# Performance work log

Hardware: AMD Instinct MI355X
Metric: run time of the kernel (lower is better)

Reference implementation:

```python
import jax, jax.numpy as jnp
import numpy as np

D_MODEL, N_HEAD, HEAD_SIZE = 1024, 16, 64
NEG_INF = -1e30


def setup_inputs() -> dict:
    key = jax.random.key(0)
    ks = jax.random.split(key, 12)
    B, S = 4, 4096
    w = 0.02
    return {
        "query": jax.random.normal(ks[0], (B, S, D_MODEL), jnp.float32),
        "key":   jax.random.normal(ks[1], (B, S, D_MODEL), jnp.float32),
        "value": jax.random.normal(ks[2], (B, S, D_MODEL), jnp.float32),
        "mask":  jnp.ones((HEAD_SIZE, HEAD_SIZE), jnp.int32),
        "Wq": jax.random.normal(ks[3], (D_MODEL, HEAD_SIZE), jnp.float32) * w,
        "bq": jnp.zeros((HEAD_SIZE,), jnp.float32),
        "Wk": jax.random.normal(ks[4], (D_MODEL, HEAD_SIZE), jnp.float32) * w,
        "bk": jnp.zeros((HEAD_SIZE,), jnp.float32),
        "Wv": jax.random.normal(ks[5], (D_MODEL, HEAD_SIZE), jnp.float32) * w,
        "bv": jnp.zeros((HEAD_SIZE,), jnp.float32),
        "Wp": jax.random.normal(ks[6], (D_MODEL, D_MODEL), jnp.float32) * w,
        "bp": jnp.zeros((D_MODEL,), jnp.float32),
    }


def reference(query, key, value, mask, Wq, bq, Wk, bk, Wv, bv, Wp, bp):
    h, dh = N_HEAD, HEAD_SIZE
    # Linear projections: (B,S,d_model) -> (B,S,head_size)
    q = query @ Wq + bq
    k = key @ Wk + bk
    v = value @ Wv + bv
    # Faithful to torch: view(-1, h, dh).transpose(1,2) on (B,S,head_size)
    # -> (N, dh, h) with N = B*S/h
    q = q.reshape(-1, h, dh).transpose(0, 2, 1)
    k = k.reshape(-1, h, dh).transpose(0, 2, 1)
    v = v.reshape(-1, h, dh).transpose(0, 2, 1)
    scale = q.shape[-1] ** (-0.5)  # dhead = h in the original code
    # scores: (N, dh, dh)
    scores = jnp.einsum('nik,njk->nij', q, k) * scale
    scores = jnp.where(mask == 0, NEG_INF, scores)
    # NOTE: original code computes softmax(scores) but then overwrites it;
    # the actual output uses dropout(raw scores) @ v. Dropout in eval = identity.
    x = jnp.einsum('nij,njh->nih', scores, v)  # (N, dh, h)
    x = x.transpose(0, 2, 1).reshape(-1, h * dh)  # (N, d_model)
    return x @ Wp + bp
```

## Files before the change

kernel.cpp:

```cpp
#include <hip/hip_runtime.h>
#include <hip/hip_bf16.h>
#include <stdint.h>


typedef float f32x4 __attribute__((ext_vector_type(4)));
typedef short s16x8 __attribute__((ext_vector_type(8)));

#define T_TOK 16384
#define KDIM  1024
#define HS    64

__device__ __forceinline__ short f2bf(float f) {
    union { float f; uint32_t u; } x; x.f = f;
    uint32_t u = x.u;
    u += 0x7FFFu + ((u >> 16) & 1u);
    return (short)(u >> 16);
}

__device__ __forceinline__ void gl2lds16(const void* g, void* l) {
    __builtin_amdgcn_global_load_lds(
        (const __attribute__((address_space(1))) void*)g,
        (__attribute__((address_space(3))) void*)l, 16, 0, 0);
}

__global__ __launch_bounds__(256) void wtrans_kernel(
    const float* __restrict__ Wq, const float* __restrict__ Wk,
    const float* __restrict__ Wv, const float* __restrict__ Wp,
    short* __restrict__ Wtq, short* __restrict__ Wtk,
    short* __restrict__ Wtv, short* __restrict__ Wpt)
{
    const int bid = blockIdx.x;
    const float* src; short* dst; int N, k0, n0;
    if (bid < 256) { src = Wp; dst = Wpt; N = 1024; k0 = (bid >> 4) * 64; n0 = (bid & 15) * 64; }
    else {
        int r = bid - 256; int p = r >> 4;
        src = (p == 0) ? Wq : (p == 1) ? Wk : Wv;
        dst = (p == 0) ? Wtq : (p == 1) ? Wtk : Wtv;
        N = 64; k0 = (r & 15) * 64; n0 = 0;
    }
    __shared__ float Ts[64][68];
    const int tid = threadIdx.x;
    #pragma unroll
    for (int i = 0; i < 4; ++i) {
        int idx = i * 256 + tid;
        int r = idx >> 4, c4 = idx & 15;
        f32x4 v = *(const f32x4*)&src[(size_t)(k0 + r) * N + n0 + c4 * 4];
        *(f32x4*)&Ts[r][c4 * 4] = v;
    }
    __syncthreads();
    #pragma unroll
    for (int i = 0; i < 2; ++i) {
        int idx = i * 256 + tid;
        int n = idx >> 3, c8 = idx & 7;
        s16x8 h;
        #pragma unroll
        for (int j = 0; j < 8; ++j) h[j] = f2bf(Ts[c8 * 8 + j][n]);
        *(s16x8*)&dst[(size_t)(n0 + n) * KDIM + k0 + c8 * 8] = h;
    }
}

__global__ __launch_bounds__(256) void qkv_proj_kernel(
    const float* __restrict__ Q, const float* __restrict__ K,
    const float* __restrict__ V,
    const short* __restrict__ Wtq, const short* __restrict__ Wtk,
    const short* __restrict__ Wtv,
    const float* __restrict__ bq, const float* __restrict__ bk,
    const float* __restrict__ bv,
    float* __restrict__ OutQKV)
{
    const int p = blockIdx.y;
    const float* In = (p == 0) ? Q : (p == 1) ? K : V;
    const short* Wt = (p == 0) ? Wtq : (p == 1) ? Wtk : Wtv;
    const float* bb = (p == 0) ? bq : (p == 1) ? bk : bv;
    float* Out = OutQKV + (size_t)p * T_TOK * HS;

    __shared__ __align__(16) char ldsA[2][4096];
    __shared__ __align__(16) char ldsB[2][8192];

    const int tid  = threadIdx.x;
    const int wave = tid >> 6;
    const int lane = tid & 63;
    const int lhi  = lane >> 4;
    const int llo  = lane & 15;
    const int t0   = blockIdx.x * 32;

    int oB0 = (wave * 2 + 0) * 1024 + lane * 16;
    int oB1 = (wave * 2 + 1) * 1024 + lane * 16;
    int rB0 = oB0 >> 7, qB0 = (oB0 >> 4) & 7;
    int rB1 = oB1 >> 7, qB1 = (oB1 >> 4) & 7;
    size_t gB0 = (size_t)rB0 * KDIM + ((qB0 ^ (rB0 & 7)) * 8);
    size_t gB1 = (size_t)rB1 * KDIM + ((qB1 ^ (rB1 & 7)) * 8);

    const int rt = tid >> 3;
    const int dg = tid & 7;
    const float* gAp = In + (size_t)(t0 + rt) * KDIM + dg * 8;
    const int aWoff = rt * 128 + ((dg ^ (rt & 7)) * 16);

    f32x4 acc[2] = {};
    f32x4 ra[2][2];

    #define STAGE_B(b, kk) do {                              \
        gl2lds16(Wt + gB0 + (kk), &ldsB[b][oB0]);            \
        gl2lds16(Wt + gB1 + (kk), &ldsB[b][oB1]);            \
    } while (0)

    #define LOADA(s, kk) do {                                \
        ra[s][0] = *(const f32x4*)(gAp + (kk));              \
        ra[s][1] = *(const f32x4*)(gAp + (kk) + 4);          \
    } while (0)

    #define WRITEA(b, s) do {                                \
        s16x8 h;                                             \
        h[0] = f2bf(ra[s][0].x); h[1] = f2bf(ra[s][0].y);    \
        h[2] = f2bf(ra[s][0].z); h[3] = f2bf(ra[s][0].w);    \
        h[4] = f2bf(ra[s][1].x); h[5] = f2bf(ra[s][1].y);    \
        h[6] = f2bf(ra[s][1].z); h[7] = f2bf(ra[s][1].w);    \
        *(s16x8*)&ldsA[b][aWoff] = h;                        \
    } while (0)

    LOADA(0, 0);
    STAGE_B(0, 0);
    WRITEA(0, 0);
    LOADA(1, 64);

    #pragma unroll
    for (int c = 0; c < 16; ++c) {
        __syncthreads();
        if (c < 15) STAGE_B((c + 1) & 1, (c + 1) * 64);
        if (c < 14) LOADA(c & 1, (c + 2) * 64);
        if (c < 15) WRITEA((c + 1) & 1, (c + 1) & 1);
        const char* Ab = (const char*)ldsA[c & 1];
        const char* Bb = (const char*)ldsB[c & 1];
        #pragma unroll
        for (int hh = 0; hh < 2; ++hh) {
            int pf = (hh * 4 + lhi) ^ (llo & 7);
            s16x8 bf = *(const s16x8*)(Bb + (wave * 16 + llo) * 128 + pf * 16);
            #pragma unroll
            for (int tt = 0; tt < 2; ++tt) {
                int r = tt * 16 + llo;
                s16x8 af = *(const s16x8*)(Ab + r * 128 + pf * 16);
                acc[tt] = __builtin_amdgcn_mfma_f32_16x16x32_bf16(af, bf, acc[tt], 0, 0, 0);
            }
        }
    }
    #undef STAGE_B
    #undef LOADA
    #undef WRITEA

    const float bias = bb[wave * 16 + llo];
    #pragma unroll
    for (int tt = 0; tt < 2; ++tt)
        #pragma unroll
        for (int r = 0; r < 4; ++r)
            Out[(size_t)(t0 + tt * 16 + lhi * 4 + r) * HS + wave * 16 + llo] = acc[tt][r] + bias;
}

__global__ __launch_bounds__(256) void group_attn_kernel(
    const float* __restrict__ QKV, short* __restrict__ Xbf)
{
    const int n = blockIdx.x;
    __shared__ float Sq[16][68];
    __shared__ float Sk[16][68];
    __shared__ float Sv[16][68];
    __shared__ float KV[16][17];

    const int tid = threadIdx.x;
    const float* qp = QKV + (size_t)n * 16 * HS;
    const float* kp = qp + (size_t)T_TOK * HS;
    const float* vp = kp + (size_t)T_TOK * HS;

    {
        int row = tid >> 4, c4 = (tid & 15) * 4;
        *(f32x4*)&Sq[row][c4] = *(const f32x4*)&qp[tid * 4];
        *(f32x4*)&Sk[row][c4] = *(const f32x4*)&kp[tid * 4];
        *(f32x4*)&Sv[row][c4] = *(const f32x4*)&vp[tid * 4];
    }
    __syncthreads();

    {
        int b = tid >> 4, a = tid & 15;
        const f32x4* kb = (const f32x4*)&Sk[b][0];
        const f32x4* va = (const f32x4*)&Sv[a][0];
        float s = 0.f;
        #pragma unroll
        for (int j = 0; j < 16; ++j) {
            f32x4 x = kb[j], y = va[j];
            s += x.x * y.x + x.y * y.y + x.z * y.z + x.w * y.w;
        }
        KV[b][a] = s * 0.25f;
    }
    __syncthreads();

    const int i = tid & 63;
    const int w = tid >> 6;
    float qv[16];
    #pragma unroll
    for (int b = 0; b < 16; ++b) qv[b] = Sq[b][i];
    #pragma unroll
    for (int u = 0; u < 4; ++u) {
        int a = u * 4 + w;
        float s = 0.f;
        #pragma unroll
        for (int b = 0; b < 16; ++b) s += qv[b] * KV[b][a];
        Xbf[(size_t)n * 1024 + a * 64 + i] = f2bf(s);
    }
}

__global__ __launch_bounds__(256) void out_proj_kernel(
    const short* __restrict__ Xbf, const short* __restrict__ Wpt,
    const float* __restrict__ bp, float* __restrict__ Out)
{
    __shared__ __align__(16) char lds[2][12288];

    const int tid  = threadIdx.x;
    const int wave = tid >> 6;
    const int lane = tid & 63;
    const int lhi  = lane >> 4, llo = lane & 15;
    const int n0   = blockIdx.x * 64;
    const int m0   = blockIdx.y * 32;

    int oA = wave * 1024 + lane * 16;
    int rA = oA >> 7, qA = (oA >> 4) & 7;
    size_t gA = (size_t)(m0 + rA) * KDIM + ((qA ^ (rA & 7)) * 8);
    int oB0 = (wave * 2 + 0) * 1024 + lane * 16;
    int oB1 = (wave * 2 + 1) * 1024 + lane * 16;
    int rB0 = oB0 >> 7, qB0 = (oB0 >> 4) & 7;
    int rB1 = oB1 >> 7, qB1 = (oB1 >> 4) & 7;
    size_t gB0 = (size_t)(n0 + rB0) * KDIM + ((qB0 ^ (rB0 & 7)) * 8);
    size_t gB1 = (size_t)(n0 + rB1) * KDIM + ((qB1 ^ (rB1 & 7)) * 8);

    f32x4 acc[2] = {};

    #define STAGE3(b, kk) do {                                    \
        gl2lds16(Xbf + gA  + (kk), &lds[b][oA]);                  \
        gl2lds16(Wpt + gB0 + (kk), &lds[b][4096 + oB0]);          \
        gl2lds16(Wpt + gB1 + (kk), &lds[b][4096 + oB1]);          \
    } while (0)

    STAGE3(0, 0);
    for (int c = 0; c < 16; ++c) {
        __syncthreads();
        if (c < 15) STAGE3((c + 1) & 1, (c + 1) * 64);
        const char* Ab = lds[c & 1];
        const char* Bb = lds[c & 1] + 4096;
        #pragma unroll
        for (int hh = 0; hh < 2; ++hh) {
            int pB = (hh * 4 + lhi) ^ (llo & 7);
            s16x8 bf = *(const s16x8*)(Bb + (wave * 16 + llo) * 128 + pB * 16);
            #pragma unroll
            for (int tt = 0; tt < 2; ++tt) {
                int r = tt * 16 + llo;
                int pA = (hh * 4 + lhi) ^ (llo & 7);
                s16x8 af = *(const s16x8*)(Ab + r * 128 + pA * 16);
                acc[tt] = __builtin_amdgcn_mfma_f32_16x16x32_bf16(af, bf, acc[tt], 0, 0, 0);
            }
        }
    }
    #undef STAGE3

    const float bias = bp[n0 + wave * 16 + llo];
    #pragma unroll
    for (int tt = 0; tt < 2; ++tt)
        #pragma unroll
        for (int r = 0; r < 4; ++r)
            Out[(size_t)(m0 + tt * 16 + lhi * 4 + r) * KDIM + n0 + wave * 16 + llo]
                = acc[tt][r] + bias;
}

extern "C" void kernel_launch(void* const* d_in, const int* in_sizes, int n_in,
                              void* d_out, int out_size, void* d_ws, size_t ws_size,
                              hipStream_t stream) {
    const float* Q  = (const float*)d_in[0];
    const float* K  = (const float*)d_in[1];
    const float* V  = (const float*)d_in[2];
    const float* Wq = (const float*)d_in[4];
    const float* bq = (const float*)d_in[5];
    const float* Wk = (const float*)d_in[6];
    const float* bk = (const float*)d_in[7];
    const float* Wv = (const float*)d_in[8];
    const float* bv = (const float*)d_in[9];
    const float* Wp = (const float*)d_in[10];
    const float* bp = (const float*)d_in[11];
    float* out = (float*)d_out;

    char* ws = (char*)d_ws;
    float* qkv = (float*)ws;
    size_t off = (size_t)3 * T_TOK * HS * sizeof(float);
    short* Xbf = (short*)(ws + off); off += (size_t)1024 * 1024 * 2;
    short* Wtq = (short*)(ws + off); off += (size_t)HS * KDIM * 2;
    short* Wtk = (short*)(ws + off); off += (size_t)HS * KDIM * 2;
    short* Wtv = (short*)(ws + off); off += (size_t)HS * KDIM * 2;
    short* Wpt = (short*)(ws + off); off += (size_t)KDIM * KDIM * 2;

    wtrans_kernel<<<dim3(304), 256, 0, stream>>>(Wq, Wk, Wv, Wp, Wtq, Wtk, Wtv, Wpt);
    qkv_proj_kernel<<<dim3(T_TOK / 32, 3), 256, 0, stream>>>(
        Q, K, V, Wtq, Wtk, Wtv, bq, bk, bv, qkv);
    group_attn_kernel<<<dim3(1024), 256, 0, stream>>>(qkv, Xbf);
    out_proj_kernel<<<dim3(16, 32), 256, 0, stream>>>(Xbf, Wpt, bp, out);
}
```

Measured before the change: 252.9 us.

## Drop LDS staging in projection GEMMs and load MFMA fragments straight from global

Both the QKV projection and output projection kernels stop staging tiles through double-buffered shared memory with barriers. Each wave instead loads its A and B fragments directly from global memory into registers, and the block tile grows to 64 rows. The aim is to remove LDS traffic and __syncthreads overhead in these memory-bound GEMMs. In exchange there is no explicit prefetch pipelining, B fragments are loaded redundantly by every wave (relying on cache), and the grids shrink, which lowers parallelism.

```diff
diff --git a/kernel.cpp b/kernel.cpp
--- a/kernel.cpp
+++ b/kernel.cpp
@@ -15,12 +15,6 @@
     uint32_t u = x.u;
     u += 0x7FFFu + ((u >> 16) & 1u);
     return (short)(u >> 16);
-}
-
-__device__ __forceinline__ void gl2lds16(const void* g, void* l) {
-    __builtin_amdgcn_global_load_lds(
-        (const __attribute__((address_space(1))) void*)g,
-        (__attribute__((address_space(3))) void*)l, 16, 0, 0);
 }
 
 __global__ __launch_bounds__(256) void wtrans_kernel(
@@ -74,85 +68,51 @@
     const float* bb = (p == 0) ? bq : (p == 1) ? bk : bv;
     float* Out = OutQKV + (size_t)p * T_TOK * HS;
 
-    __shared__ __align__(16) char ldsA[2][4096];
-    __shared__ __align__(16) char ldsB[2][8192];
-
     const int tid  = threadIdx.x;
     const int wave = tid >> 6;
     const int lane = tid & 63;
     const int lhi  = lane >> 4;
     const int llo  = lane & 15;
-    const int t0   = blockIdx.x * 32;
-
-    int oB0 = (wave * 2 + 0) * 1024 + lane * 16;
-    int oB1 = (wave * 2 + 1) * 1024 + lane * 16;
-    int rB0 = oB0 >> 7, qB0 = (oB0 >> 4) & 7;
-    int rB1 = oB1 >> 7, qB1 = (oB1 >> 4) & 7;
-    size_t gB0 = (size_t)rB0 * KDIM + ((qB0 ^ (rB0 & 7)) * 8);
-    size_t gB1 = (size_t)rB1 * KDIM + ((qB1 ^ (rB1 & 7)) * 8);
-
-    const int rt = tid >> 3;
-    const int dg = tid & 7;
-    const float* gAp = In + (size_t)(t0 + rt) * KDIM + dg * 8;
-    const int aWoff = rt * 128 + ((dg ^ (rt & 7)) * 16);
-
-    f32x4 acc[2] = {};
-    f32x4 ra[2][2];
-
-    #define STAGE_B(b, kk) do {                              \
-        gl2lds16(Wt + gB0 + (kk), &ldsB[b][oB0]);            \
-        gl2lds16(Wt + gB1 + (kk), &ldsB[b][oB1]);            \
-    } while (0)
-
-    #define LOADA(s, kk) do {                                \
-        ra[s][0] = *(const f32x4*)(gAp + (kk));              \
-        ra[s][1] = *(const f32x4*)(gAp + (kk) + 4);          \
-    } while (0)
-
-    #define WRITEA(b, s) do {                                \
-        s16x8 h;                                             \
-        h[0] = f2bf(ra[s][0].x); h[1] = f2bf(ra[s][0].y);    \
-        h[2] = f2bf(ra[s][0].z); h[3] = f2bf(ra[s][0].w);    \
-        h[4] = f2bf(ra[s][1].x); h[5] = f2bf(ra[s][1].y);    \
-        h[6] = f2bf(ra[s][1].z); h[7] = f2bf(ra[s][1].w);    \
-        *(s16x8*)&ldsA[b][aWoff] = h;                        \
-    } while (0)
-
-    LOADA(0, 0);
-    STAGE_B(0, 0);
-    WRITEA(0, 0);
-    LOADA(1, 64);
+    const int t0   = blockIdx.x * 64;
+
+    const float* Ap = In + (size_t)(t0 + wave * 16 + llo) * KDIM + lhi * 8;
+    const short* Bp = Wt + (size_t)llo * KDIM + lhi * 8;
+
+    f32x4 acc[4] = {};
 
     #pragma unroll
     for (int c = 0; c < 16; ++c) {
-        __syncthreads();
-        if (c < 15) STAGE_B((c + 1) & 1, (c + 1) * 64);
-        if (c < 14) LOADA(c & 1, (c + 2) * 64);
-        if (c < 15) WRITEA((c + 1) & 1, (c + 1) & 1);
-        const char* Ab = (const char*)ldsA[c & 1];
-        const char* Bb = (const char*)ldsB[c & 1];
-        #pragma unroll
-        for (int hh = 0; hh < 2; ++hh) {
-            int pf = (hh * 4 + lhi) ^ (llo & 7);
-            s16x8 bf = *(const s16x8*)(Bb + (wave * 16 + llo) * 128 + pf * 16);
+        const int k0 = c * 64;
+        f32x4 a0l = *(const f32x4*)(Ap + k0);
+        f32x4 a0h = *(const f32x4*)(Ap + k0 + 4);
+        f32x4 a1l = *(const f32x4*)(Ap + k0 + 32);
+        f32x4 a1h = *(const f32x4*)(Ap + k0 + 36);
+        s16x8 bfr[2][4];
+        #pragma unroll
+        for (int hh = 0; hh < 2; ++hh)
             #pragma unroll
-            for (int tt = 0; tt < 2; ++tt) {
-                int r = tt * 16 + llo;
-                s16x8 af = *(const s16x8*)(Ab + r * 128 + pf * 16);
-                acc[tt] = __builtin_amdgcn_mfma_f32_16x16x32_bf16(af, bf, acc[tt], 0, 0, 0);
-            }
-        }
-    }
-    #undef STAGE_B
-    #undef LOADA
-    #undef WRITEA
-
-    const float bias = bb[wave * 16 + llo];
-    #pragma unroll
-    for (int tt = 0; tt < 2; ++tt)
+            for (int nb = 0; nb < 4; ++nb)
+                bfr[hh][nb] = *(const s16x8*)(Bp + (size_t)nb * 16 * KDIM + k0 + hh * 32);
+        s16x8 af0, af1;
+        af0[0] = f2bf(a0l.x); af0[1] = f2bf(a0l.y); af0[2] = f2bf(a0l.z); af0[3] = f2bf(a0l.w);
+        af0[4] = f2bf(a0h.x); af0[5] = f2bf(a0h.y); af0[6] = f2bf(a0h.z); af0[7] = f2bf(a0h.w);
+        af1[0] = f2bf(a1l.x); af1[1] = f2bf(a1l.y); af1[2] = f2bf(a1l.z); af1[3] = f2bf(a1l.w);
+        af1[4] = f2bf(a1h.x); af1[5] = f2bf(a1h.y); af1[6] = f2bf(a1h.z); af1[7] = f2bf(a1h.w);
+        #pragma unroll
+        for (int nb = 0; nb < 4; ++nb)
+            acc[nb] = __builtin_amdgcn_mfma_f32_16x16x32_bf16(af0, bfr[0][nb], acc[nb], 0, 0, 0);
+        #pragma unroll
+        for (int nb = 0; nb < 4; ++nb)
+            acc[nb] = __builtin_amdgcn_mfma_f32_16x16x32_bf16(af1, bfr[1][nb], acc[nb], 0, 0, 0);
+    }
+
+    #pragma unroll
+    for (int nb = 0; nb < 4; ++nb) {
+        const float bias = bb[nb * 16 + llo];
         #pragma unroll
         for (int r = 0; r < 4; ++r)
-            Out[(size_t)(t0 + tt * 16 + lhi * 4 + r) * HS + wave * 16 + llo] = acc[tt][r] + bias;
+            Out[(size_t)(t0 + wave * 16 + lhi * 4 + r) * HS + nb * 16 + llo] = acc[nb][r] + bias;
+    }
 }
 
 __global__ __launch_bounds__(256) void group_attn_kernel(
@@ -210,61 +170,45 @@
     const short* __restrict__ Xbf, const short* __restrict__ Wpt,
     const float* __restrict__ bp, float* __restrict__ Out)
 {
-    __shared__ __align__(16) char lds[2][12288];
-
     const int tid  = threadIdx.x;
     const int wave = tid >> 6;
     const int lane = tid & 63;
     const int lhi  = lane >> 4, llo = lane & 15;
     const int n0   = blockIdx.x * 64;
-    const int m0   = blockIdx.y * 32;
-
-    int oA = wave * 1024 + lane * 16;
-    int rA = oA >> 7, qA = (oA >> 4) & 7;
-    size_t gA = (size_t)(m0 + rA) * KDIM + ((qA ^ (rA & 7)) * 8);
-    int oB0 = (wave * 2 + 0) * 1024 + lane * 16;
-    int oB1 = (wave * 2 + 1) * 1024 + lane * 16;
-    int rB0 = oB0 >> 7, qB0 = (oB0 >> 4) & 7;
-    int rB1 = oB1 >> 7, qB1 = (oB1 >> 4) & 7;
-    size_t gB0 = (size_t)(n0 + rB0) * KDIM + ((qB0 ^ (rB0 & 7)) * 8);
-    size_t gB1 = (size_t)(n0 + rB1) * KDIM + ((qB1 ^ (rB1 & 7)) * 8);
-
-    f32x4 acc[2] = {};
-
-    #define STAGE3(b, kk) do {                                    \
-        gl2lds16(Xbf + gA  + (kk), &lds[b][oA]);                  \
-        gl2lds16(Wpt + gB0 + (kk), &lds[b][4096 + oB0]);          \
-        gl2lds16(Wpt + gB1 + (kk), &lds[b][4096 + oB1]);          \
-    } while (0)
-
-    STAGE3(0, 0);
+    const int m0   = blockIdx.y * 64;
+
+    const short* Ap = Xbf + (size_t)(m0 + wave * 16 + llo) * KDIM + lhi * 8;
+    const short* Bp = Wpt + (size_t)(n0 + llo) * KDIM + lhi * 8;
+
+    f32x4 acc[4] = {};
+
+    #pragma unroll
     for (int c = 0; c < 16; ++c) {
-        __syncthreads();
-        if (c < 15) STAGE3((c + 1) & 1, (c + 1) * 64);
-        const char* Ab = lds[c & 1];
-        const char* Bb = lds[c & 1] + 4096;
-        #pragma unroll
-        for (int hh = 0; hh < 2; ++hh) {
-            int pB = (hh * 4 + lhi) ^ (llo & 7);
-            s16x8 bf = *(const s16x8*)(Bb + (wave * 16 + llo) * 128 + pB * 16);
+        const int k0 = c * 64;
+        s16x8 af0 = *(const s16x8*)(Ap + k0);
+        s16x8 af1 = *(const s16x8*)(Ap + k0 + 32);
+        s16x8 bfr[2][4];
+        #pragma unroll
+        for (int hh = 0; hh < 2; ++hh)
             #pragma unroll
-            for (int tt = 0; tt < 2; ++tt) {
-                int r = tt * 16 + llo;
-                int pA = (hh * 4 + lhi) ^ (llo & 7);
-                s16x8 af = *(const s16x8*)(Ab + r * 128 + pA * 16);
-                acc[tt] = __builtin_amdgcn_mfma_f32_16x16x32_bf16(af, bf, acc[tt], 0, 0, 0);
-            }
-        }
-    }
-    #undef STAGE3
-
-    const float bias = bp[n0 + wave * 16 + llo];
-    #pragma unroll
-    for (int tt = 0; tt < 2; ++tt)
+            for (int nb = 0; nb < 4; ++nb)
+                bfr[hh][nb] = *(const s16x8*)(Bp + (size_t)nb * 16 * KDIM + k0 + hh * 32);
+        #pragma unroll
+        for (int nb = 0; nb < 4; ++nb)
+            acc[nb] = __builtin_amdgcn_mfma_f32_16x16x32_bf16(af0, bfr[0][nb], acc[nb], 0, 0, 0);
+        #pragma unroll
+        for (int nb = 0; nb < 4; ++nb)
+            acc[nb] = __builtin_amdgcn_mfma_f32_16x16x32_bf16(af1, bfr[1][nb], acc[nb], 0, 0, 0);
+    }
+
+    #pragma unroll
+    for (int nb = 0; nb < 4; ++nb) {
+        const float bias = bp[n0 + nb * 16 + llo];
         #pragma unroll
         for (int r = 0; r < 4; ++r)
-            Out[(size_t)(m0 + tt * 16 + lhi * 4 + r) * KDIM + n0 + wave * 16 + llo]
-                = acc[tt][r] + bias;
+            Out[(size_t)(m0 + wave * 16 + lhi * 4 + r) * KDIM + n0 + nb * 16 + llo]
+                = acc[nb][r] + bias;
+    }
 }
 
 extern "C" void kernel_launch(void* const* d_in, const int* in_sizes, int n_in,
@@ -293,8 +237,8 @@
     short* Wpt = (short*)(ws + off); off += (size_t)KDIM * KDIM * 2;
 
     wtrans_kernel<<<dim3(304), 256, 0, stream>>>(Wq, Wk, Wv, Wp, Wtq, Wtk, Wtv, Wpt);
-    qkv_proj_kernel<<<dim3(T_TOK / 32, 3), 256, 0, stream>>>(
+    qkv_proj_kernel<<<dim3(T_TOK / 64, 3), 256, 0, stream>>>(
         Q, K, V, Wtq, Wtk, Wtv, bq, bk, bv, qkv);
     group_attn_kernel<<<dim3(1024), 256, 0, stream>>>(qkv, Xbf);
-    out_proj_kernel<<<dim3(16, 32), 256, 0, stream>>>(Xbf, Wpt, bp, out);
-}
+    out_proj_kernel<<<dim3(16, 16), 256, 0, stream>>>(Xbf, Wpt, bp, out);
+}
```

Measured after the change: 268.1 us. +6.0%, slower.
